# Kernel optimization log

Hardware: AMD Instinct MI355X
Metric: run time of the kernel (lower is better)

Reference implementation:

```python
import jax, jax.numpy as jnp
import numpy as np

L, B, C = 512, 64, 512  # seq_len, batch, tags_size


def setup_inputs() -> dict:
    key = jax.random.key(0)
    k1, k2, k3, k4, k5, k6 = jax.random.split(key, 6)
    std = (1.0 / C) ** 0.5
    emit = jax.random.normal(k1, (L, B, C), dtype=jnp.float32)
    trans = jax.random.normal(k2, (C, C), dtype=jnp.float32) * std
    trans_from_start = jax.random.normal(k3, (C,), dtype=jnp.float32) * std
    trans_to_end = jax.random.normal(k4, (C,), dtype=jnp.float32) * std
    target = jax.random.randint(k5, (L, B), 0, C)
    # left-aligned length mask so mask.sum(0)-1 indexes the last valid step
    lens = jax.random.randint(k6, (B,), L // 2, L + 1)
    mask = jnp.arange(L)[:, None] < lens[None, :]
    return {"emit": emit, "target": target, "mask": mask, "trans": trans,
            "trans_from_start": trans_from_start, "trans_to_end": trans_to_end}


def _log_z(emit, mask, trans, trans_from_start, trans_to_end):
    log_alpha0 = emit[0] + trans_from_start  # (B, C)

    def step(log_alpha, xs):
        e_i, m_i = xs  # (B, C), (B,)
        # scores[b, j] = logsumexp_i( log_alpha[b, i] + trans[i, j] + e_i[b, j] )
        s = jax.nn.logsumexp(log_alpha[:, :, None] + trans[None, :, :] + e_i[:, None, :], axis=1)
        log_alpha = jnp.where(m_i[:, None], s, log_alpha)
        return log_alpha, None

    log_alpha, _ = jax.lax.scan(step, log_alpha0, (emit[1:], mask[1:]))
    return jax.nn.logsumexp(log_alpha + trans_to_end, axis=1).sum()


def _score(emit, target, mask, trans, trans_from_start, trans_to_end):
    l, b, c = emit.shape
    tr = trans[target[:-1], target[1:]]  # (L-1, B)
    scores = jnp.concatenate([jnp.zeros((1, b), emit.dtype), tr], axis=0)
    scores = scores + jnp.take_along_axis(emit, target[:, :, None], axis=2)[..., 0]
    score = jnp.where(mask, scores, jnp.zeros((), emit.dtype)).sum()
    ends = mask.sum(axis=0) - 1  # (B,) index of last valid step
    last_tags = target[ends, jnp.arange(b)]
    score = score + trans_from_start[target[0]].sum() + trans_to_end[last_tags].sum()
    return score


def reference(emit, target, mask, trans, trans_from_start, trans_to_end):
    b = emit.shape[1]
    log_z = _log_z(emit, mask, trans, trans_from_start, trans_to_end)
    score = _score(emit, target, mask, trans, trans_from_start, trans_to_end)
    return (log_z - score) / b
```

## Files before the change

kernel.cpp:

```cpp
#include <hip/hip_runtime.h>
#include <hip/hip_bf16.h>
#include <stdint.h>

#define LL 512
#define BB 64
#define CC 512
#define TM 255

typedef float float4v __attribute__((ext_vector_type(4)));
typedef int   int4v   __attribute__((ext_vector_type(4)));
typedef int   int8v   __attribute__((ext_vector_type(8)));

#define WS_ET     262144
#define WS_SCORE  524288
#define WS_SVA    524292
#define WS_SVB    524548
#define WS_ALPHA  528384
#define WS_BETA   659456


__device__ __forceinline__ bool mask_at(const void* maskp, bool is_byte, int t, int b) {
    if (is_byte) return ((const unsigned char*)maskp)[t * BB + b] != 0;
    return ((const int*)maskp)[t * BB + b] != 0;
}

__device__ __forceinline__ float rowmax16_dpp(float x) {
    int t;
    t = __builtin_amdgcn_update_dpp(0, __float_as_int(x), 0x128, 0xF, 0xF, true);
    x = fmaxf(x, __int_as_float(t));
    t = __builtin_amdgcn_update_dpp(0, __float_as_int(x), 0x124, 0xF, 0xF, true);
    x = fmaxf(x, __int_as_float(t));
    t = __builtin_amdgcn_update_dpp(0, __float_as_int(x), 0x122, 0xF, 0xF, true);
    x = fmaxf(x, __int_as_float(t));
    t = __builtin_amdgcn_update_dpp(0, __float_as_int(x), 0x121, 0xF, 0xF, true);
    x = fmaxf(x, __int_as_float(t));
    return x;
}

__global__ void prep_kernel(const float* __restrict__ trans, unsigned char* __restrict__ ws) {
    int g = blockIdx.x * blockDim.x + threadIdx.x;
    if (g == 0) *(float*)(ws + WS_SCORE) = 0.0f;
    if (g >= 512 * 128) return;
    int n  = g & 511;
    int pd = g >> 9;
    int wv = pd >> 4, rw = pd & 15;
    float f[4], ft[4];
#pragma unroll
    for (int nt = 0; nt < 4; ++nt) {
        int k = 64 * wv + 16 * nt + rw;
        f[nt]  = __expf(trans[(size_t)k * CC + n]);
        ft[nt] = __expf(trans[(size_t)n * CC + k]);
    }
    int r = 0;
    r = __builtin_amdgcn_cvt_pk_fp8_f32(f[0], f[1], r, false);
    r = __builtin_amdgcn_cvt_pk_fp8_f32(f[2], f[3], r, true);
    ((int*)ws)[n * 128 + pd] = r;
    int r2 = 0;
    r2 = __builtin_amdgcn_cvt_pk_fp8_f32(ft[0], ft[1], r2, false);
    r2 = __builtin_amdgcn_cvt_pk_fp8_f32(ft[2], ft[3], r2, true);
    ((int*)(ws + WS_ET))[n * 128 + pd] = r2;
}

__launch_bounds__(512, 2)
__global__ void crf_scan_kernel(const float* __restrict__ emit,
                                const int* __restrict__ target,
                                const void* __restrict__ maskp,
                                const float* __restrict__ trans,
                                const float* __restrict__ tfs,
                                const float* __restrict__ t2e,
                                unsigned char* __restrict__ ws) {
    const int tid = threadIdx.x;
    const bool is_byte = ((const unsigned char*)maskp)[1] != 0;

    if (blockIdx.x >= 8) {
        int sb = blockIdx.x - 8;
        float val = 0.0f;
        for (int e = sb * 512 + tid; e < LL * BB; e += 32 * 512) {
            int t = e >> 6, b = e & 63;
            if (mask_at(maskp, is_byte, t, b)) {
                int tg  = target[t * BB + b];
                float v = emit[(size_t)(t * BB + b) * CC + tg];
                if (t > 0) v += trans[(size_t)target[(t - 1) * BB + b] * CC + tg];
                val += v;
            }
        }
        if (sb == 0 && tid < BB) {
            int b = tid;
            val += tfs[target[b]];
            int lo = 0, hi = LL;
            while (lo < hi) {
                int mid = (lo + hi) >> 1;
                if (mask_at(maskp, is_byte, mid, b)) lo = mid + 1; else hi = mid;
            }
            val += t2e[target[(lo - 1) * BB + b]];
        }
        for (int off = 32; off > 0; off >>= 1) val += __shfl_down(val, off);
        if ((tid & 63) == 0) atomicAdd((float*)(ws + WS_SCORE), val);
        return;
    }

    const bool is_fwd = blockIdx.x < 4;
    const int B0 = (is_fwd ? blockIdx.x : blockIdx.x - 4) * 16;

    __shared__ __align__(16) unsigned char p8[2][16 * 528];
    __shared__ float mslot[4][16];
    __shared__ float Sv[16];
    __shared__ float m0S[16];
    __shared__ float red[16][32];
    __shared__ int   lenS[16];
    __shared__ float mInitS;

    const int wv   = tid >> 6;
    const int lane = tid & 63;
    const int q    = lane >> 4;
    const int r15  = lane & 15;

    const unsigned char* ews = ws + (is_fwd ? 0 : WS_ET);
    int8v ef[4][4];
#pragma unroll
    for (int nt = 0; nt < 4; ++nt) {
        int n = (wv * 4 + nt) * 16 + r15;
#pragma unroll
        for (int kk4 = 0; kk4 < 4; ++kk4) {
            const unsigned char* src = ews + n * 512 + kk4 * 128 + q * 32;
            int4v lo = *(const int4v*)(src);
            int4v hi = *(const int4v*)(src + 16);
            ef[nt][kk4] = __builtin_shufflevector(lo, hi, 0, 1, 2, 3, 4, 5, 6, 7);
        }
    }

    const int c5 = tid >> 5;
    const int s5 = tid & 31;

    if (is_fwd) {
        {
            float lmax = -3.0e38f;
#pragma unroll
            for (int i = 0; i < 4; ++i) {
                int j4 = s5 + 32 * i;
                float4v em = *(const float4v*)(emit + (size_t)(B0 + c5) * CC + 4 * j4);
                float4v tf = *(const float4v*)(tfs + 4 * j4);
                float4v a = em + tf;
                lmax = fmaxf(lmax, fmaxf(fmaxf(a.x, a.y), fmaxf(a.z, a.w)));
            }
            red[c5][s5] = lmax;
        }
        __syncthreads();
        if (tid < 16) {
            float m0 = red[tid][0];
            for (int s = 1; s < 32; ++s) m0 = fmaxf(m0, red[tid][s]);
            Sv[tid]  = m0;
            m0S[tid] = m0;
            mslot[0][tid] = 1.0f;
            mslot[1][tid] = 0.0f;
            mslot[2][tid] = 0.0f;
            mslot[3][tid] = 0.0f;
        }
        __syncthreads();
        {
            float m0 = m0S[c5];
#pragma unroll
            for (int i = 0; i < 4; ++i) {
                int pd = s5 + 32 * i;
                int wvv = pd >> 4, rw = pd & 15;
                float f[4];
#pragma unroll
                for (int nt = 0; nt < 4; ++nt) {
                    int k = 64 * wvv + 16 * nt + rw;
                    f[nt] = __expf(emit[(size_t)(B0 + c5) * CC + k] + tfs[k] - m0);
                }
                int r = 0;
                r = __builtin_amdgcn_cvt_pk_fp8_f32(f[0], f[1], r, false);
                r = __builtin_amdgcn_cvt_pk_fp8_f32(f[2], f[3], r, true);
                *(int*)(&p8[0][0] + c5 * 528 + pd * 4) = r;
            }
        }
        __syncthreads();
    } else {
        {
            float m = t2e[tid];
            for (int off = 32; off > 0; off >>= 1) m = fmaxf(m, __shfl_xor(m, off));
            if (lane == 0) ((float*)red)[wv] = m;
        }
        if (tid < 16) {
            Sv[tid] = 0.0f;
            mslot[0][tid] = 0.0f;
            mslot[1][tid] = 0.0f;
            mslot[2][tid] = 0.0f;
            mslot[3][tid] = 0.0f;
        }
        __syncthreads();
        if (tid == 0) {
            float m = ((float*)red)[0];
            for (int i = 1; i < 8; ++i) m = fmaxf(m, ((float*)red)[i]);
            mInitS = __expf(m);
        }
        __syncthreads();
        {
#pragma unroll
            for (int i = 0; i < 4; ++i) {
                int pd = s5 + 32 * i;
                int wvv = pd >> 4, rw = pd & 15;
                float f[4];
#pragma unroll
                for (int nt = 0; nt < 4; ++nt)
                    f[nt] = __expf(t2e[64 * wvv + 16 * nt + rw]);
                int r = 0;
                r = __builtin_amdgcn_cvt_pk_fp8_f32(f[0], f[1], r, false);
                r = __builtin_amdgcn_cvt_pk_fp8_f32(f[2], f[3], r, true);
                *(int*)(&p8[0][0] + c5 * 528 + pd * 4) = r;
                *(int*)(&p8[1][0] + c5 * 528 + pd * 4) = r;
            }
            int part = 0;
            for (int k = 0; k < 16; ++k)
                part += mask_at(maskp, is_byte, s5 * 16 + k, B0 + c5) ? 1 : 0;
            red[c5][s5] = (float)part;
        }
        __syncthreads();
        if (tid < 16) {
            int s = 0;
            for (int i = 0; i < 32; ++i) s += (int)red[tid][i];
            lenS[tid] = s;
        }
        __syncthreads();
    }

    int lenR[4] = {LL, LL, LL, LL};
    float mInit = 0.0f;
    if (!is_fwd) {
#pragma unroll
        for (int rr = 0; rr < 4; ++rr) lenR[rr] = lenS[q * 4 + rr];
        mInit = mInitS;
    }
    float et2e[4];
#pragma unroll
    for (int nt = 0; nt < 4; ++nt)
        et2e[nt] = __expf(t2e[(wv * 4 + nt) * 16 + r15]);
    float rQ[4] = {1.0f, 1.0f, 1.0f, 1.0f};

    if (is_fwd) {
        const float* eb0 = emit + (size_t)(BB + B0 + q * 4) * CC + (wv * 64 + r15);
        const float* eb1 = eb0 + 2 * CC;
        float ex[16];
#pragma unroll
        for (int nt = 0; nt < 4; ++nt)
#pragma unroll
            for (int rr = 0; rr < 2; ++rr) {
                ex[nt * 4 + rr]     = __expf(eb0[rr * CC + nt * 16]);
                ex[nt * 4 + rr + 2] = __expf(eb1[rr * CC + nt * 16]);
            }

#pragma unroll 2
        for (int t = 1; t <= TM; ++t) {
            const int wp = t & 1;
            const int rp = wp ^ 1;

            const int step = (t < TM) ? (BB * CC) : 0;
            float emn[16];
#pragma unroll
            for (int nt = 0; nt < 4; ++nt)
#pragma unroll
                for (int rr = 0; rr < 2; ++rr) {
                    emn[nt * 4 + rr]     = eb0[step + rr * CC + nt * 16];
                    emn[nt * 4 + rr + 2] = eb1[step + rr * CC + nt * 16];
                }

            int8v af[4];
            const unsigned char* pr = &p8[rp][0] + r15 * 528 + q * 32;
#pragma unroll
            for (int kk4 = 0; kk4 < 4; ++kk4) {
                int4v lo = *(const int4v*)(pr + kk4 * 128);
                int4v hi = *(const int4v*)(pr + kk4 * 128 + 16);
                af[kk4] = __builtin_shufflevector(lo, hi, 0, 1, 2, 3, 4, 5, 6, 7);
            }

            float sig[4], rcv[4];
#pragma unroll
            for (int rr = 0; rr < 4; ++rr) {
                float M1 = mslot[(t - 1) & 3][q * 4 + rr];
                sig[rr] = 64.0f * M1 * rQ[rr];
                rcv[rr] = 1.0f / sig[rr];
                rQ[rr]  = rcv[rr];
            }

            if (wv == 0 && r15 == 0) {
#pragma unroll
                for (int rr = 0; rr < 4; ++rr) mslot[(t + 1) & 3][q * 4 + rr] = 0.0f;
            }

            float4v acc[4];
            const float4v z = {0.f, 0.f, 0.f, 0.f};
#pragma unroll
            for (int nt = 0; nt < 4; ++nt) acc[nt] = z;

#pragma unroll
            for (int kk4 = 0; kk4 < 4; ++kk4)
#pragma unroll
                for (int nt = 0; nt < 2; ++nt)
                    acc[nt] = __builtin_amdgcn_mfma_scale_f32_16x16x128_f8f6f4(
                        af[kk4], ef[nt][kk4], acc[nt],
                        0, 0, 0, 0x7F7F7F7F, 0, 0x7F7F7F7F);

            float exn[16];
#pragma unroll
            for (int i = 0; i < 16; ++i) exn[i] = __expf(emn[i]);

#pragma unroll
            for (int kk4 = 0; kk4 < 4; ++kk4)
#pragma unroll
                for (int nt = 2; nt < 4; ++nt)
                    acc[nt] = __builtin_amdgcn_mfma_scale_f32_16x16x128_f8f6f4(
                        af[kk4], ef[nt][kk4], acc[nt],
                        0, 0, 0, 0x7F7F7F7F, 0, 0x7F7F7F7F);

            float rowmax[4];
#pragma unroll
            for (int rr = 0; rr < 4; ++rr) {
                float v0 = acc[0][rr] * ex[0 * 4 + rr];
                float v1 = acc[1][rr] * ex[1 * 4 + rr];
                acc[0][rr] = v0; acc[1][rr] = v1;
                rowmax[rr] = fmaxf(v0, v1);
            }
#pragma unroll
            for (int rr = 0; rr < 4; ++rr) {
                float v2 = acc[2][rr] * ex[2 * 4 + rr];
                float v3 = acc[3][rr] * ex[3 * 4 + rr];
                acc[2][rr] = v2; acc[3][rr] = v3;
                rowmax[rr] = fmaxf(rowmax[rr], fmaxf(v2, v3));
            }

            {
                unsigned char* wrow = &p8[wp][0] + (wv * 16 + r15) * 4;
#pragma unroll
                for (int rr = 0; rr < 4; ++rr) {
                    float p0 = fminf(acc[0][rr] * rcv[rr], 448.0f);
                    float p1 = fminf(acc[1][rr] * rcv[rr], 448.0f);
                    float p2 = fminf(acc[2][rr] * rcv[rr], 448.0f);
                    float p3 = fminf(acc[3][rr] * rcv[rr], 448.0f);
                    int r = 0;
                    r = __builtin_amdgcn_cvt_pk_fp8_f32(p0, p1, r, false);
                    r = __builtin_amdgcn_cvt_pk_fp8_f32(p2, p3, r, true);
                    *(int*)(wrow + (q * 4 + rr) * 528) = r;
                }
            }

#pragma unroll
            for (int rr = 0; rr < 4; ++rr) {
                float mr = rowmax16_dpp(rowmax[rr]);
                if (r15 == 0)
                    atomicMax((int*)&mslot[t & 3][q * 4 + rr], __float_as_int(mr));
            }

            if (wv == 0 && r15 == 0) {
#pragma unroll
                for (int rr = 0; rr < 4; ++rr) Sv[q * 4 + rr] += __logf(sig[rr]);
            }

            if (t == TM) {
                float* wA = (float*)(ws + WS_ALPHA) + (size_t)(B0 + q * 4) * CC + (wv * 64 + r15);
#pragma unroll
                for (int rr = 0; rr < 4; ++rr)
#pragma unroll
                    for (int nt = 0; nt < 4; ++nt)
                        wA[(size_t)rr * CC + nt * 16] = acc[nt][rr] * rcv[rr];
            }

#pragma unroll
            for (int i = 0; i < 16; ++i) ex[i] = exn[i];
            eb0 += BB * CC;
            eb1 += BB * CC;
            __syncthreads();
        }
        if (tid < 16) ((float*)(ws + WS_SVA))[B0 + tid] = Sv[tid];
    } else {
        const float* eb0 = emit + ((size_t)(LL - 1) * BB + B0 + q * 4) * CC + (wv * 64 + r15);
        const float* eb1 = eb0 + 2 * CC;
        float ex[16];
#pragma unroll
        for (int nt = 0; nt < 4; ++nt)
#pragma unroll
            for (int rr = 0; rr < 2; ++rr) {
                ex[nt * 4 + rr]     = __expf(eb0[rr * CC + nt * 16]);
                ex[nt * 4 + rr + 2] = __expf(eb1[rr * CC + nt * 16]);
            }

#pragma unroll 2
        for (int it = 0; it < 256; ++it) {
            const int t  = 510 - it;
            const int wp = it & 1;
            const int rp = wp ^ 1;

            const int step = (it < 255) ? -(BB * CC) : 0;
            float emn[16];
#pragma unroll
            for (int nt = 0; nt < 4; ++nt)
#pragma unroll
                for (int rr = 0; rr < 2; ++rr) {
                    emn[nt * 4 + rr]     = eb0[step + rr * CC + nt * 16];
                    emn[nt * 4 + rr + 2] = eb1[step + rr * CC + nt * 16];
                }

            int8v af[4];
            const unsigned char* pr = &p8[rp][0] + r15 * 528 + q * 32;
#pragma unroll
            for (int kk4 = 0; kk4 < 4; ++kk4) {
                int4v lo = *(const int4v*)(pr + kk4 * 128);
                int4v hi = *(const int4v*)(pr + kk4 * 128 + 16);
                af[kk4] = __builtin_shufflevector(lo, hi, 0, 1, 2, 3, 4, 5, 6, 7);
            }

            float sig[4], rcv[4];
#pragma unroll
            for (int rr = 0; rr < 4; ++rr) {
                bool ui  = (t >= lenR[rr] - 2);
                float M1 = ui ? mInit : mslot[(it + 3) & 3][q * 4 + rr];
                float rq = ui ? 1.0f : rQ[rr];
                sig[rr] = 64.0f * M1 * rq;
                rcv[rr] = 1.0f / sig[rr];
                rQ[rr]  = rcv[rr];
            }

            if (wv == 0 && r15 == 0) {
#pragma unroll
                for (int rr = 0; rr < 4; ++rr) mslot[(it + 1) & 3][q * 4 + rr] = 0.0f;
            }

            float4v acc[4];
            const float4v z = {0.f, 0.f, 0.f, 0.f};
#pragma unroll
            for (int nt = 0; nt < 4; ++nt) acc[nt] = z;

#pragma unroll
            for (int kk4 = 0; kk4 < 4; ++kk4)
#pragma unroll
                for (int nt = 0; nt < 2; ++nt)
                    acc[nt] = __builtin_amdgcn_mfma_scale_f32_16x16x128_f8f6f4(
                        af[kk4], ef[nt][kk4], acc[nt],
                        0, 0, 0, 0x7F7F7F7F, 0, 0x7F7F7F7F);

            float exn[16];
#pragma unroll
            for (int i = 0; i < 16; ++i) exn[i] = __expf(emn[i]);

#pragma unroll
            for (int kk4 = 0; kk4 < 4; ++kk4)
#pragma unroll
                for (int nt = 2; nt < 4; ++nt)
                    acc[nt] = __builtin_amdgcn_mfma_scale_f32_16x16x128_f8f6f4(
                        af[kk4], ef[nt][kk4], acc[nt],
                        0, 0, 0, 0x7F7F7F7F, 0, 0x7F7F7F7F);

            float rowmax[4];
#pragma unroll
            for (int rr = 0; rr < 4; ++rr) {
                float v0 = acc[0][rr] * ex[0 * 4 + rr];
                float v1 = acc[1][rr] * ex[1 * 4 + rr];
                acc[0][rr] = v0; acc[1][rr] = v1;
                rowmax[rr] = fmaxf(v0, v1);
            }
#pragma unroll
            for (int rr = 0; rr < 4; ++rr) {
                float v2 = acc[2][rr] * ex[2 * 4 + rr];
                float v3 = acc[3][rr] * ex[3 * 4 + rr];
                acc[2][rr] = v2; acc[3][rr] = v3;
                rowmax[rr] = fmaxf(rowmax[rr], fmaxf(v2, v3));
            }

            {
                unsigned char* wrow = &p8[wp][0] + (wv * 16 + r15) * 4;
#pragma unroll
                for (int rr = 0; rr < 4; ++rr) {
                    float p0 = fminf(acc[0][rr] * rcv[rr], 448.0f);
                    float p1 = fminf(acc[1][rr] * rcv[rr], 448.0f);
                    float p2 = fminf(acc[2][rr] * rcv[rr], 448.0f);
                    float p3 = fminf(acc[3][rr] * rcv[rr], 448.0f);
                    int r = 0;
                    r = __builtin_amdgcn_cvt_pk_fp8_f32(p0, p1, r, false);
                    r = __builtin_amdgcn_cvt_pk_fp8_f32(p2, p3, r, true);
                    if (t <= lenR[rr] - 2)
                        *(int*)(wrow + (q * 4 + rr) * 528) = r;
                }
            }

#pragma unroll
            for (int rr = 0; rr < 4; ++rr) {
                float mr = rowmax16_dpp(rowmax[rr]);
                if (r15 == 0)
                    atomicMax((int*)&mslot[it & 3][q * 4 + rr], __float_as_int(mr));
            }

            if (wv == 0 && r15 == 0) {
#pragma unroll
                for (int rr = 0; rr < 4; ++rr)
                    if (t <= lenR[rr] - 2) Sv[q * 4 + rr] += __logf(sig[rr]);
            }

            if (t == TM) {
                float* wB = (float*)(ws + WS_BETA) + (size_t)(B0 + q * 4) * CC + (wv * 64 + r15);
#pragma unroll
                for (int rr = 0; rr < 4; ++rr) {
                    bool live = (t <= lenR[rr] - 2);
#pragma unroll
                    for (int nt = 0; nt < 4; ++nt)
                        wB[(size_t)rr * CC + nt * 16] = live ? (acc[nt][rr] * rcv[rr]) : et2e[nt];
                }
            }

#pragma unroll
            for (int i = 0; i < 16; ++i) ex[i] = exn[i];
            eb0 -= BB * CC;
            eb1 -= BB * CC;
            __syncthreads();
        }
        if (tid < 16) ((float*)(ws + WS_SVB))[B0 + tid] = Sv[tid];
    }
}

__global__ void combine_kernel(const unsigned char* __restrict__ ws, float* __restrict__ out) {
    __shared__ float acc8[8];
    const int tid = threadIdx.x;
    const int c  = tid >> 3;
    const int s8 = tid & 7;
    const float* A = (const float*)(ws + WS_ALPHA) + (size_t)c * CC;
    const float* B = (const float*)(ws + WS_BETA)  + (size_t)c * CC;
    float d = 0.0f;
    for (int i = s8; i < CC; i += 8) d += A[i] * B[i];
    d += __shfl_xor(d, 1);
    d += __shfl_xor(d, 2);
    d += __shfl_xor(d, 4);
    float v = 0.0f;
    if (s8 == 0)
        v = ((const float*)(ws + WS_SVA))[c] + ((const float*)(ws + WS_SVB))[c] + __logf(d);
    for (int off = 32; off > 0; off >>= 1) v += __shfl_down(v, off);
    if ((tid & 63) == 0) acc8[tid >> 6] = v;
    __syncthreads();
    if (tid == 0) {
        float s = 0.0f;
        for (int i = 0; i < 8; ++i) s += acc8[i];
        out[0] = (s - *(const float*)(ws + WS_SCORE)) * (1.0f / 64.0f);
    }
}

extern "C" void kernel_launch(void* const* d_in, const int* in_sizes, int n_in,
                              void* d_out, int out_size, void* d_ws, size_t ws_size,
                              hipStream_t stream) {
    const float* emit   = (const float*)d_in[0];
    const int*   target = (const int*)d_in[1];
    const void*  maskp  = d_in[2];
    const float* trans  = (const float*)d_in[3];
    const float* tfs    = (const float*)d_in[4];
    const float* t2e    = (const float*)d_in[5];
    unsigned char* ws   = (unsigned char*)d_ws;
    float* out          = (float*)d_out;

    prep_kernel<<<256, 256, 0, stream>>>(trans, ws);
    crf_scan_kernel<<<40, 512, 0, stream>>>(emit, target, maskp, trans, tfs, t2e, ws);
    combine_kernel<<<1, 512, 0, stream>>>(ws, out);
}
```

Baseline: 534.1 us.

## Split scan columns across 16 waves with 1024-thread blocks

The forward and backward scan blocks now launch 1024 threads instead of 512, so each wave owns 32 output columns (2 MFMA tiles) instead of 64. This halves the dependent MFMA chain and the exp work each wave does per time step. To match the new column ownership, the fp8 probability write-back uses a remapped byte offset with 2-byte stores, and the score reduction blocks are resized to 16 blocks of 1024 threads. The cost is a block-wide barrier across twice as many waves every step, higher per-block register pressure under the new launch bounds, and loop unrolling is turned off.

```diff
diff --git a/kernel.cpp b/kernel.cpp
--- a/kernel.cpp
+++ b/kernel.cpp
@@ -61,7 +61,7 @@
     ((int*)(ws + WS_ET))[n * 128 + pd] = r2;
 }
 
-__launch_bounds__(512, 2)
+__launch_bounds__(1024, 1)
 __global__ void crf_scan_kernel(const float* __restrict__ emit,
                                 const int* __restrict__ target,
                                 const void* __restrict__ maskp,
@@ -75,7 +75,7 @@
     if (blockIdx.x >= 8) {
         int sb = blockIdx.x - 8;
         float val = 0.0f;
-        for (int e = sb * 512 + tid; e < LL * BB; e += 32 * 512) {
+        for (int e = sb * 1024 + tid; e < LL * BB; e += 16 * 1024) {
             int t = e >> 6, b = e & 63;
             if (mask_at(maskp, is_byte, t, b)) {
                 int tg  = target[t * BB + b];
@@ -116,10 +116,10 @@
     const int r15  = lane & 15;
 
     const unsigned char* ews = ws + (is_fwd ? 0 : WS_ET);
-    int8v ef[4][4];
-#pragma unroll
-    for (int nt = 0; nt < 4; ++nt) {
-        int n = (wv * 4 + nt) * 16 + r15;
+    int8v ef[2][4];
+#pragma unroll
+    for (int nt = 0; nt < 2; ++nt) {
+        int n = wv * 32 + nt * 16 + r15;
 #pragma unroll
         for (int kk4 = 0; kk4 < 4; ++kk4) {
             const unsigned char* src = ews + n * 512 + kk4 * 128 + q * 32;
@@ -133,7 +133,7 @@
     const int s5 = tid & 31;
 
     if (is_fwd) {
-        {
+        if (tid < 512) {
             float lmax = -3.0e38f;
 #pragma unroll
             for (int i = 0; i < 4; ++i) {
@@ -157,7 +157,7 @@
             mslot[3][tid] = 0.0f;
         }
         __syncthreads();
-        {
+        if (tid < 512) {
             float m0 = m0S[c5];
 #pragma unroll
             for (int i = 0; i < 4; ++i) {
@@ -177,7 +177,7 @@
         }
         __syncthreads();
     } else {
-        {
+        if (tid < 512) {
             float m = t2e[tid];
             for (int off = 32; off > 0; off >>= 1) m = fmaxf(m, __shfl_xor(m, off));
             if (lane == 0) ((float*)red)[wv] = m;
@@ -196,7 +196,7 @@
             mInitS = __expf(m);
         }
         __syncthreads();
-        {
+        if (tid < 512) {
 #pragma unroll
             for (int i = 0; i < 4; ++i) {
                 int pd = s5 + 32 * i;
@@ -225,54 +225,42 @@
         __syncthreads();
     }
 
-    int lenR[4] = {LL, LL, LL, LL};
-    float mInit = 0.0f;
-    if (!is_fwd) {
-#pragma unroll
-        for (int rr = 0; rr < 4; ++rr) lenR[rr] = lenS[q * 4 + rr];
-        mInit = mInitS;
-    }
-    float et2e[4];
-#pragma unroll
-    for (int nt = 0; nt < 4; ++nt)
-        et2e[nt] = __expf(t2e[(wv * 4 + nt) * 16 + r15]);
     float rQ[4] = {1.0f, 1.0f, 1.0f, 1.0f};
+    const int wcol = (wv >> 1) * 64 + r15 * 4 + (wv & 1) * 2;
 
     if (is_fwd) {
-        const float* eb0 = emit + (size_t)(BB + B0 + q * 4) * CC + (wv * 64 + r15);
+        const float* eb0 = emit + (size_t)(BB + B0 + q * 4) * CC + (wv * 32 + r15);
         const float* eb1 = eb0 + 2 * CC;
-        float ex[16];
-#pragma unroll
-        for (int nt = 0; nt < 4; ++nt)
+        float ex[8];
+#pragma unroll
+        for (int nt = 0; nt < 2; ++nt)
 #pragma unroll
             for (int rr = 0; rr < 2; ++rr) {
                 ex[nt * 4 + rr]     = __expf(eb0[rr * CC + nt * 16]);
                 ex[nt * 4 + rr + 2] = __expf(eb1[rr * CC + nt * 16]);
             }
 
-#pragma unroll 2
+#pragma unroll 1
         for (int t = 1; t <= TM; ++t) {
             const int wp = t & 1;
             const int rp = wp ^ 1;
 
             const int step = (t < TM) ? (BB * CC) : 0;
-            float emn[16];
-#pragma unroll
-            for (int nt = 0; nt < 4; ++nt)
+            float emn[8];
+#pragma unroll
+            for (int nt = 0; nt < 2; ++nt)
 #pragma unroll
                 for (int rr = 0; rr < 2; ++rr) {
                     emn[nt * 4 + rr]     = eb0[step + rr * CC + nt * 16];
                     emn[nt * 4 + rr + 2] = eb1[step + rr * CC + nt * 16];
                 }
 
-            int8v af[4];
             const unsigned char* pr = &p8[rp][0] + r15 * 528 + q * 32;
-#pragma unroll
-            for (int kk4 = 0; kk4 < 4; ++kk4) {
-                int4v lo = *(const int4v*)(pr + kk4 * 128);
-                int4v hi = *(const int4v*)(pr + kk4 * 128 + 16);
-                af[kk4] = __builtin_shufflevector(lo, hi, 0, 1, 2, 3, 4, 5, 6, 7);
-            }
+            int8v af0, af1, af2, af3;
+            { int4v lo = *(const int4v*)(pr + 0 * 128); int4v hi = *(const int4v*)(pr + 0 * 128 + 16);
+              af0 = __builtin_shufflevector(lo, hi, 0, 1, 2, 3, 4, 5, 6, 7); }
+            { int4v lo = *(const int4v*)(pr + 1 * 128); int4v hi = *(const int4v*)(pr + 1 * 128 + 16);
+              af1 = __builtin_shufflevector(lo, hi, 0, 1, 2, 3, 4, 5, 6, 7); }
 
             float sig[4], rcv[4];
 #pragma unroll
@@ -282,65 +270,48 @@
                 rcv[rr] = 1.0f / sig[rr];
                 rQ[rr]  = rcv[rr];
             }
-
             if (wv == 0 && r15 == 0) {
 #pragma unroll
                 for (int rr = 0; rr < 4; ++rr) mslot[(t + 1) & 3][q * 4 + rr] = 0.0f;
             }
 
-            float4v acc[4];
             const float4v z = {0.f, 0.f, 0.f, 0.f};
-#pragma unroll
-            for (int nt = 0; nt < 4; ++nt) acc[nt] = z;
-
-#pragma unroll
-            for (int kk4 = 0; kk4 < 4; ++kk4)
-#pragma unroll
-                for (int nt = 0; nt < 2; ++nt)
-                    acc[nt] = __builtin_amdgcn_mfma_scale_f32_16x16x128_f8f6f4(
-                        af[kk4], ef[nt][kk4], acc[nt],
-                        0, 0, 0, 0x7F7F7F7F, 0, 0x7F7F7F7F);
-
-            float exn[16];
-#pragma unroll
-            for (int i = 0; i < 16; ++i) exn[i] = __expf(emn[i]);
-
-#pragma unroll
-            for (int kk4 = 0; kk4 < 4; ++kk4)
-#pragma unroll
-                for (int nt = 2; nt < 4; ++nt)
-                    acc[nt] = __builtin_amdgcn_mfma_scale_f32_16x16x128_f8f6f4(
-                        af[kk4], ef[nt][kk4], acc[nt],
-                        0, 0, 0, 0x7F7F7F7F, 0, 0x7F7F7F7F);
+            float4v acc0 = z, acc1 = z;
+            acc0 = __builtin_amdgcn_mfma_scale_f32_16x16x128_f8f6f4(af0, ef[0][0], acc0, 0, 0, 0, 0x7F7F7F7F, 0, 0x7F7F7F7F);
+            acc1 = __builtin_amdgcn_mfma_scale_f32_16x16x128_f8f6f4(af0, ef[1][0], acc1, 0, 0, 0, 0x7F7F7F7F, 0, 0x7F7F7F7F);
+            { int4v lo = *(const int4v*)(pr + 2 * 128); int4v hi = *(const int4v*)(pr + 2 * 128 + 16);
+              af2 = __builtin_shufflevector(lo, hi, 0, 1, 2, 3, 4, 5, 6, 7); }
+            { int4v lo = *(const int4v*)(pr + 3 * 128); int4v hi = *(const int4v*)(pr + 3 * 128 + 16);
+              af3 = __builtin_shufflevector(lo, hi, 0, 1, 2, 3, 4, 5, 6, 7); }
+            acc0 = __builtin_amdgcn_mfma_scale_f32_16x16x128_f8f6f4(af1, ef[0][1], acc0, 0, 0, 0, 0x7F7F7F7F, 0, 0x7F7F7F7F);
+            acc1 = __builtin_amdgcn_mfma_scale_f32_16x16x128_f8f6f4(af1, ef[1][1], acc1, 0, 0, 0, 0x7F7F7F7F, 0, 0x7F7F7F7F);
+
+            float exn[8];
+#pragma unroll
+            for (int i = 0; i < 8; ++i) exn[i] = __expf(emn[i]);
+
+            acc0 = __builtin_amdgcn_mfma_scale_f32_16x16x128_f8f6f4(af2, ef[0][2], acc0, 0, 0, 0, 0x7F7F7F7F, 0, 0x7F7F7F7F);
+            acc1 = __builtin_amdgcn_mfma_scale_f32_16x16x128_f8f6f4(af2, ef[1][2], acc1, 0, 0, 0, 0x7F7F7F7F, 0, 0x7F7F7F7F);
+            acc0 = __builtin_amdgcn_mfma_scale_f32_16x16x128_f8f6f4(af3, ef[0][3], acc0, 0, 0, 0, 0x7F7F7F7F, 0, 0x7F7F7F7F);
+            acc1 = __builtin_amdgcn_mfma_scale_f32_16x16x128_f8f6f4(af3, ef[1][3], acc1, 0, 0, 0, 0x7F7F7F7F, 0, 0x7F7F7F7F);
 
             float rowmax[4];
 #pragma unroll
             for (int rr = 0; rr < 4; ++rr) {
-                float v0 = acc[0][rr] * ex[0 * 4 + rr];
-                float v1 = acc[1][rr] * ex[1 * 4 + rr];
-                acc[0][rr] = v0; acc[1][rr] = v1;
+                float v0 = acc0[rr] * ex[rr];
+                float v1 = acc1[rr] * ex[4 + rr];
+                acc0[rr] = v0; acc1[rr] = v1;
                 rowmax[rr] = fmaxf(v0, v1);
             }
-#pragma unroll
-            for (int rr = 0; rr < 4; ++rr) {
-                float v2 = acc[2][rr] * ex[2 * 4 + rr];
-                float v3 = acc[3][rr] * ex[3 * 4 + rr];
-                acc[2][rr] = v2; acc[3][rr] = v3;
-                rowmax[rr] = fmaxf(rowmax[rr], fmaxf(v2, v3));
-            }
 
             {
-                unsigned char* wrow = &p8[wp][0] + (wv * 16 + r15) * 4;
+                unsigned char* wbase = &p8[wp][0] + wcol;
 #pragma unroll
                 for (int rr = 0; rr < 4; ++rr) {
-                    float p0 = fminf(acc[0][rr] * rcv[rr], 448.0f);
-                    float p1 = fminf(acc[1][rr] * rcv[rr], 448.0f);
-                    float p2 = fminf(acc[2][rr] * rcv[rr], 448.0f);
-                    float p3 = fminf(acc[3][rr] * rcv[rr], 448.0f);
-                    int r = 0;
-                    r = __builtin_amdgcn_cvt_pk_fp8_f32(p0, p1, r, false);
-                    r = __builtin_amdgcn_cvt_pk_fp8_f32(p2, p3, r, true);
-                    *(int*)(wrow + (q * 4 + rr) * 528) = r;
+                    float p0 = fminf(acc0[rr] * rcv[rr], 448.0f);
+                    float p1 = fminf(acc1[rr] * rcv[rr], 448.0f);
+                    int r = __builtin_amdgcn_cvt_pk_fp8_f32(p0, p1, 0, false);
+                    *(short*)(wbase + (q * 4 + rr) * 528) = (short)r;
                 }
             }
 
@@ -357,57 +328,60 @@
             }
 
             if (t == TM) {
-                float* wA = (float*)(ws + WS_ALPHA) + (size_t)(B0 + q * 4) * CC + (wv * 64 + r15);
-#pragma unroll
-                for (int rr = 0; rr < 4; ++rr)
-#pragma unroll
-                    for (int nt = 0; nt < 4; ++nt)
-                        wA[(size_t)rr * CC + nt * 16] = acc[nt][rr] * rcv[rr];
-            }
-
-#pragma unroll
-            for (int i = 0; i < 16; ++i) ex[i] = exn[i];
+                float* wA = (float*)(ws + WS_ALPHA) + (size_t)(B0 + q * 4) * CC + (wv * 32 + r15);
+#pragma unroll
+                for (int rr = 0; rr < 4; ++rr) {
+                    wA[(size_t)rr * CC + 0]  = acc0[rr] * rcv[rr];
+                    wA[(size_t)rr * CC + 16] = acc1[rr] * rcv[rr];
+                }
+            }
+
+#pragma unroll
+            for (int i = 0; i < 8; ++i) ex[i] = exn[i];
             eb0 += BB * CC;
             eb1 += BB * CC;
             __syncthreads();
         }
         if (tid < 16) ((float*)(ws + WS_SVA))[B0 + tid] = Sv[tid];
     } else {
-        const float* eb0 = emit + ((size_t)(LL - 1) * BB + B0 + q * 4) * CC + (wv * 64 + r15);
+        int lenR[4];
+        float mInit = mInitS;
+#pragma unroll
+        for (int rr = 0; rr < 4; ++rr) lenR[rr] = lenS[q * 4 + rr];
+
+        const float* eb0 = emit + ((size_t)(LL - 1) * BB + B0 + q * 4) * CC + (wv * 32 + r15);
         const float* eb1 = eb0 + 2 * CC;
-        float ex[16];
-#pragma unroll
-        for (int nt = 0; nt < 4; ++nt)
+        float ex[8];
+#pragma unroll
+        for (int nt = 0; nt < 2; ++nt)
 #pragma unroll
             for (int rr = 0; rr < 2; ++rr) {
                 ex[nt * 4 + rr]     = __expf(eb0[rr * CC + nt * 16]);
                 ex[nt * 4 + rr + 2] = __expf(eb1[rr * CC + nt * 16]);
             }
 
-#pragma unroll 2
+#pragma unroll 1
         for (int it = 0; it < 256; ++it) {
             const int t  = 510 - it;
             const int wp = it & 1;
             const int rp = wp ^ 1;
 
             const int step = (it < 255) ? -(BB * CC) : 0;
-            float emn[16];
-#pragma unroll
-            for (int nt = 0; nt < 4; ++nt)
+            float emn[8];
+#pragma unroll
+            for (int nt = 0; nt < 2; ++nt)
 #pragma unroll
                 for (int rr = 0; rr < 2; ++rr) {
                     emn[nt * 4 + rr]     = eb0[step + rr * CC + nt * 16];
                     emn[nt * 4 + rr + 2] = eb1[step + rr * CC + nt * 16];
                 }
 
-            int8v af[4];
             const unsigned char* pr = &p8[rp][0] + r15 * 528 + q * 32;
-#pragma unroll
-            for (int kk4 = 0; kk4 < 4; ++kk4) {
-                int4v lo = *(const int4v*)(pr + kk4 * 128);
-                int4v hi = *(const int4v*)(pr + kk4 * 128 + 16);
-                af[kk4] = __builtin_shufflevector(lo, hi, 0, 1, 2, 3, 4, 5, 6, 7);
-            }
+            int8v af0, af1, af2, af3;
+            { int4v lo = *(const int4v*)(pr + 0 * 128); int4v hi = *(const int4v*)(pr + 0 * 128 + 16);
+              af0 = __builtin_shufflevector(lo, hi, 0, 1, 2, 3, 4, 5, 6, 7); }
+            { int4v lo = *(const int4v*)(pr + 1 * 128); int4v hi = *(const int4v*)(pr + 1 * 128 + 16);
+              af1 = __builtin_shufflevector(lo, hi, 0, 1, 2, 3, 4, 5, 6, 7); }
 
             float sig[4], rcv[4];
 #pragma unroll
@@ -419,66 +393,49 @@
                 rcv[rr] = 1.0f / sig[rr];
                 rQ[rr]  = rcv[rr];
             }
-
             if (wv == 0 && r15 == 0) {
 #pragma unroll
                 for (int rr = 0; rr < 4; ++rr) mslot[(it + 1) & 3][q * 4 + rr] = 0.0f;
             }
 
-            float4v acc[4];
             const float4v z = {0.f, 0.f, 0.f, 0.f};
-#pragma unroll
-            for (int nt = 0; nt < 4; ++nt) acc[nt] = z;
-
-#pragma unroll
-            for (int kk4 = 0; kk4 < 4; ++kk4)
-#pragma unroll
-                for (int nt = 0; nt < 2; ++nt)
-                    acc[nt] = __builtin_amdgcn_mfma_scale_f32_16x16x128_f8f6f4(
-                        af[kk4], ef[nt][kk4], acc[nt],
-                        0, 0, 0, 0x7F7F7F7F, 0, 0x7F7F7F7F);
-
-            float exn[16];
-#pragma unroll
-            for (int i = 0; i < 16; ++i) exn[i] = __expf(emn[i]);
-
-#pragma unroll
-            for (int kk4 = 0; kk4 < 4; ++kk4)
-#pragma unroll
-                for (int nt = 2; nt < 4; ++nt)
-                    acc[nt] = __builtin_amdgcn_mfma_scale_f32_16x16x128_f8f6f4(
-                        af[kk4], ef[nt][kk4], acc[nt],
-                        0, 0, 0, 0x7F7F7F7F, 0, 0x7F7F7F7F);
+            float4v acc0 = z, acc1 = z;
+            acc0 = __builtin_amdgcn_mfma_scale_f32_16x16x128_f8f6f4(af0, ef[0][0], acc0, 0, 0, 0, 0x7F7F7F7F, 0, 0x7F7F7F7F);
+            acc1 = __builtin_amdgcn_mfma_scale_f32_16x16x128_f8f6f4(af0, ef[1][0], acc1, 0, 0, 0, 0x7F7F7F7F, 0, 0x7F7F7F7F);
+            { int4v lo = *(const int4v*)(pr + 2 * 128); int4v hi = *(const int4v*)(pr + 2 * 128 + 16);
+              af2 = __builtin_shufflevector(lo, hi, 0, 1, 2, 3, 4, 5, 6, 7); }
+            { int4v lo = *(const int4v*)(pr + 3 * 128); int4v hi = *(const int4v*)(pr + 3 * 128 + 16);
+              af3 = __builtin_shufflevector(lo, hi, 0, 1, 2, 3, 4, 5, 6, 7); }
+            acc0 = __builtin_amdgcn_mfma_scale_f32_16x16x128_f8f6f4(af1, ef[0][1], acc0, 0, 0, 0, 0x7F7F7F7F, 0, 0x7F7F7F7F);
+            acc1 = __builtin_amdgcn_mfma_scale_f32_16x16x128_f8f6f4(af1, ef[1][1], acc1, 0, 0, 0, 0x7F7F7F7F, 0, 0x7F7F7F7F);
+
+            float exn[8];
+#pragma unroll
+            for (int i = 0; i < 8; ++i) exn[i] = __expf(emn[i]);
+
+            acc0 = __builtin_amdgcn_mfma_scale_f32_16x16x128_f8f6f4(af2, ef[0][2], acc0, 0, 0, 0, 0x7F7F7F7F, 0, 0x7F7F7F7F);
+            acc1 = __builtin_amdgcn_mfma_scale_f32_16x16x128_f8f6f4(af2, ef[1][2], acc1, 0, 0, 0, 0x7F7F7F7F, 0, 0x7F7F7F7F);
+            acc0 = __builtin_amdgcn_mfma_scale_f32_16x16x128_f8f6f4(af3, ef[0][3], acc0, 0, 0, 0, 0x7F7F7F7F, 0, 0x7F7F7F7F);
+            acc1 = __builtin_amdgcn_mfma_scale_f32_16x16x128_f8f6f4(af3, ef[1][3], acc1, 0, 0, 0, 0x7F7F7F7F, 0, 0x7F7F7F7F);
 
             float rowmax[4];
 #pragma unroll
             for (int rr = 0; rr < 4; ++rr) {
-                float v0 = acc[0][rr] * ex[0 * 4 + rr];
-                float v1 = acc[1][rr] * ex[1 * 4 + rr];
-                acc[0][rr] = v0; acc[1][rr] = v1;
+                float v0 = acc0[rr] * ex[rr];
+                float v1 = acc1[rr] * ex[4 + rr];
+                acc0[rr] = v0; acc1[rr] = v1;
                 rowmax[rr] = fmaxf(v0, v1);
             }
-#pragma unroll
-            for (int rr = 0; rr < 4; ++rr) {
-                float v2 = acc[2][rr] * ex[2 * 4 + rr];
-                float v3 = acc[3][rr] * ex[3 * 4 + rr];
-                acc[2][rr] = v2; acc[3][rr] = v3;
-                rowmax[rr] = fmaxf(rowmax[rr], fmaxf(v2, v3));
-            }
 
             {
-                unsigned char* wrow = &p8[wp][0] + (wv * 16 + r15) * 4;
+                unsigned char* wbase = &p8[wp][0] + wcol;
 #pragma unroll
                 for (int rr = 0; rr < 4; ++rr) {
-                    float p0 = fminf(acc[0][rr] * rcv[rr], 448.0f);
-                    float p1 = fminf(acc[1][rr] * rcv[rr], 448.0f);
-                    float p2 = fminf(acc[2][rr] * rcv[rr], 448.0f);
-                    float p3 = fminf(acc[3][rr] * rcv[rr], 448.0f);
-                    int r = 0;
-                    r = __builtin_amdgcn_cvt_pk_fp8_f32(p0, p1, r, false);
-                    r = __builtin_amdgcn_cvt_pk_fp8_f32(p2, p3, r, true);
+                    float p0 = fminf(acc0[rr] * rcv[rr], 448.0f);
+                    float p1 = fminf(acc1[rr] * rcv[rr], 448.0f);
+                    int r = __builtin_amdgcn_cvt_pk_fp8_f32(p0, p1, 0, false);
                     if (t <= lenR[rr] - 2)
-                        *(int*)(wrow + (q * 4 + rr) * 528) = r;
+                        *(short*)(wbase + (q * 4 + rr) * 528) = (short)r;
                 }
             }
 
@@ -496,18 +453,19 @@
             }
 
             if (t == TM) {
-                float* wB = (float*)(ws + WS_BETA) + (size_t)(B0 + q * 4) * CC + (wv * 64 + r15);
+                float* wB = (float*)(ws + WS_BETA) + (size_t)(B0 + q * 4) * CC + (wv * 32 + r15);
+                float e0 = __expf(t2e[wv * 32 + r15]);
+                float e1 = __expf(t2e[wv * 32 + 16 + r15]);
 #pragma unroll
                 for (int rr = 0; rr < 4; ++rr) {
                     bool live = (t <= lenR[rr] - 2);
-#pragma unroll
-                    for (int nt = 0; nt < 4; ++nt)
-                        wB[(size_t)rr * CC + nt * 16] = live ? (acc[nt][rr] * rcv[rr]) : et2e[nt];
-                }
-            }
-
-#pragma unroll
-            for (int i = 0; i < 16; ++i) ex[i] = exn[i];
+                    wB[(size_t)rr * CC + 0]  = live ? (acc0[rr] * rcv[rr]) : e0;
+                    wB[(size_t)rr * CC + 16] = live ? (acc1[rr] * rcv[rr]) : e1;
+                }
+            }
+
+#pragma unroll
+            for (int i = 0; i < 8; ++i) ex[i] = exn[i];
             eb0 -= BB * CC;
             eb1 -= BB * CC;
             __syncthreads();
@@ -554,6 +512,6 @@
     float* out          = (float*)d_out;
 
     prep_kernel<<<256, 256, 0, stream>>>(trans, ws);
-    crf_scan_kernel<<<40, 512, 0, stream>>>(emit, target, maskp, trans, tfs, t2e, ws);
+    crf_scan_kernel<<<24, 1024, 0, stream>>>(emit, target, maskp, trans, tfs, t2e, ws);
     combine_kernel<<<1, 512, 0, stream>>>(ws, out);
 }
```

After: 1.119 ms. 110% more time.

## Use power-of-two exponent rescaling and a lighter barrier in the CRF recurrence

Applied to the files above, without the earlier changes.

Replaces the per-step float rescale (reciprocal of 64*max times the previous factor, plus a logf accumulated in shared memory) with a power-of-two scale built directly from the max's exponent bits. The log-normaliser is kept as an integer exponent sum in registers. It also vectorises the elementwise scale, clamp and max work, moves the emission pointer advance and load ahead, and swaps __syncthreads for a custom lgkmcnt-wait plus s_barrier. This removes a division, a log and shared-memory traffic from the serial critical path. The cost is coarser scaling granularity, which changes the fp8 range usage, and a hand-rolled barrier that depends on correct wait-count semantics.

```diff
diff --git a/kernel.cpp b/kernel.cpp
--- a/kernel.cpp
+++ b/kernel.cpp
@@ -35,6 +35,26 @@
     t = __builtin_amdgcn_update_dpp(0, __float_as_int(x), 0x121, 0xF, 0xF, true);
     x = fmaxf(x, __int_as_float(t));
     return x;
+}
+
+__device__ __forceinline__ float4v vmax4(float4v a, float4v b) {
+    float4v r;
+    r[0] = fmaxf(a[0], b[0]); r[1] = fmaxf(a[1], b[1]);
+    r[2] = fmaxf(a[2], b[2]); r[3] = fmaxf(a[3], b[3]);
+    return r;
+}
+__device__ __forceinline__ float4v vmin4s(float4v a, float c) {
+    float4v r;
+    r[0] = fminf(a[0], c); r[1] = fminf(a[1], c);
+    r[2] = fminf(a[2], c); r[3] = fminf(a[3], c);
+    return r;
+}
+
+__device__ __forceinline__ void step_barrier() {
+    asm volatile("s_waitcnt lgkmcnt(0)" ::: "memory");
+    __builtin_amdgcn_sched_barrier(0);
+    __builtin_amdgcn_s_barrier();
+    asm volatile("" ::: "memory");
 }
 
 __global__ void prep_kernel(const float* __restrict__ trans, unsigned char* __restrict__ ws) {
@@ -103,8 +123,7 @@
     const int B0 = (is_fwd ? blockIdx.x : blockIdx.x - 4) * 16;
 
     __shared__ __align__(16) unsigned char p8[2][16 * 528];
-    __shared__ float mslot[4][16];
-    __shared__ float Sv[16];
+    __shared__ __align__(16) float mslot[4][16];
     __shared__ float m0S[16];
     __shared__ float red[16][32];
     __shared__ int   lenS[16];
@@ -149,7 +168,6 @@
         if (tid < 16) {
             float m0 = red[tid][0];
             for (int s = 1; s < 32; ++s) m0 = fmaxf(m0, red[tid][s]);
-            Sv[tid]  = m0;
             m0S[tid] = m0;
             mslot[0][tid] = 1.0f;
             mslot[1][tid] = 0.0f;
@@ -183,7 +201,6 @@
             if (lane == 0) ((float*)red)[wv] = m;
         }
         if (tid < 16) {
-            Sv[tid] = 0.0f;
             mslot[0][tid] = 0.0f;
             mslot[1][tid] = 0.0f;
             mslot[2][tid] = 0.0f;
@@ -225,73 +242,59 @@
         __syncthreads();
     }
 
-    int lenR[4] = {LL, LL, LL, LL};
-    float mInit = 0.0f;
-    if (!is_fwd) {
-#pragma unroll
-        for (int rr = 0; rr < 4; ++rr) lenR[rr] = lenS[q * 4 + rr];
-        mInit = mInitS;
-    }
-    float et2e[4];
-#pragma unroll
-    for (int nt = 0; nt < 4; ++nt)
-        et2e[nt] = __expf(t2e[(wv * 4 + nt) * 16 + r15]);
-    float rQ[4] = {1.0f, 1.0f, 1.0f, 1.0f};
+    int4v gsum = {0, 0, 0, 0};
+    const float4v z4 = {0.f, 0.f, 0.f, 0.f};
 
     if (is_fwd) {
         const float* eb0 = emit + (size_t)(BB + B0 + q * 4) * CC + (wv * 64 + r15);
         const float* eb1 = eb0 + 2 * CC;
-        float ex[16];
-#pragma unroll
-        for (int nt = 0; nt < 4; ++nt)
-#pragma unroll
-            for (int rr = 0; rr < 2; ++rr) {
-                ex[nt * 4 + rr]     = __expf(eb0[rr * CC + nt * 16]);
-                ex[nt * 4 + rr + 2] = __expf(eb1[rr * CC + nt * 16]);
-            }
+        float4v ex4[4];
+#pragma unroll
+        for (int nt = 0; nt < 4; ++nt) {
+            ex4[nt][0] = __expf(eb0[0 * CC + nt * 16]);
+            ex4[nt][1] = __expf(eb0[1 * CC + nt * 16]);
+            ex4[nt][2] = __expf(eb1[0 * CC + nt * 16]);
+            ex4[nt][3] = __expf(eb1[1 * CC + nt * 16]);
+        }
 
 #pragma unroll 2
         for (int t = 1; t <= TM; ++t) {
             const int wp = t & 1;
             const int rp = wp ^ 1;
-
-            const int step = (t < TM) ? (BB * CC) : 0;
-            float emn[16];
-#pragma unroll
-            for (int nt = 0; nt < 4; ++nt)
-#pragma unroll
-                for (int rr = 0; rr < 2; ++rr) {
-                    emn[nt * 4 + rr]     = eb0[step + rr * CC + nt * 16];
-                    emn[nt * 4 + rr + 2] = eb1[step + rr * CC + nt * 16];
-                }
-
+            eb0 += BB * CC;
+            eb1 += BB * CC;
+
+            const unsigned char* pr = &p8[rp][0] + r15 * 528 + q * 32;
             int8v af[4];
-            const unsigned char* pr = &p8[rp][0] + r15 * 528 + q * 32;
 #pragma unroll
             for (int kk4 = 0; kk4 < 4; ++kk4) {
                 int4v lo = *(const int4v*)(pr + kk4 * 128);
                 int4v hi = *(const int4v*)(pr + kk4 * 128 + 16);
                 af[kk4] = __builtin_shufflevector(lo, hi, 0, 1, 2, 3, 4, 5, 6, 7);
             }
-
-            float sig[4], rcv[4];
-#pragma unroll
-            for (int rr = 0; rr < 4; ++rr) {
-                float M1 = mslot[(t - 1) & 3][q * 4 + rr];
-                sig[rr] = 64.0f * M1 * rQ[rr];
-                rcv[rr] = 1.0f / sig[rr];
-                rQ[rr]  = rcv[rr];
-            }
-
-            if (wv == 0 && r15 == 0) {
-#pragma unroll
-                for (int rr = 0; rr < 4; ++rr) mslot[(t + 1) & 3][q * 4 + rr] = 0.0f;
-            }
+            int4v me = *(const int4v*)&mslot[(t - 1) & 3][q * 4];
+
+            float4v emn4[4];
+#pragma unroll
+            for (int nt = 0; nt < 4; ++nt) {
+                emn4[nt][0] = eb0[0 * CC + nt * 16];
+                emn4[nt][1] = eb0[1 * CC + nt * 16];
+                emn4[nt][2] = eb1[0 * CC + nt * 16];
+                emn4[nt][3] = eb1[1 * CC + nt * 16];
+            }
+
+            int4v e4 = me >> 23;
+            int4v s2b = (248 - e4) << 23;
+            float4v s24;
+            s24[0] = __int_as_float(s2b[0]); s24[1] = __int_as_float(s2b[1]);
+            s24[2] = __int_as_float(s2b[2]); s24[3] = __int_as_float(s2b[3]);
+
+            if (wv == 0 && r15 == 0)
+                *(float4v*)&mslot[(t + 1) & 3][q * 4] = z4;
 
             float4v acc[4];
-            const float4v z = {0.f, 0.f, 0.f, 0.f};
-#pragma unroll
-            for (int nt = 0; nt < 4; ++nt) acc[nt] = z;
+#pragma unroll
+            for (int nt = 0; nt < 4; ++nt) acc[nt] = z4;
 
 #pragma unroll
             for (int kk4 = 0; kk4 < 4; ++kk4)
@@ -301,9 +304,14 @@
                         af[kk4], ef[nt][kk4], acc[nt],
                         0, 0, 0, 0x7F7F7F7F, 0, 0x7F7F7F7F);
 
-            float exn[16];
-#pragma unroll
-            for (int i = 0; i < 16; ++i) exn[i] = __expf(emn[i]);
+            float4v exn4[4];
+#pragma unroll
+            for (int nt = 0; nt < 4; ++nt) {
+                exn4[nt][0] = __expf(emn4[nt][0]);
+                exn4[nt][1] = __expf(emn4[nt][1]);
+                exn4[nt][2] = __expf(emn4[nt][2]);
+                exn4[nt][3] = __expf(emn4[nt][3]);
+            }
 
 #pragma unroll
             for (int kk4 = 0; kk4 < 4; ++kk4)
@@ -313,122 +321,117 @@
                         af[kk4], ef[nt][kk4], acc[nt],
                         0, 0, 0, 0x7F7F7F7F, 0, 0x7F7F7F7F);
 
-            float rowmax[4];
+            float4v p4[4];
+#pragma unroll
+            for (int nt = 0; nt < 4; ++nt) {
+                float4v exr = ex4[nt] * s24;
+                p4[nt] = acc[nt] * exr;
+            }
+
+            if (t == TM) {
+                float* wA = (float*)(ws + WS_ALPHA) + (size_t)(B0 + q * 4) * CC + (wv * 64 + r15);
+#pragma unroll
+                for (int nt = 0; nt < 4; ++nt)
+#pragma unroll
+                    for (int rr = 0; rr < 4; ++rr)
+                        wA[(size_t)rr * CC + nt * 16] = p4[nt][rr];
+            }
+
+            float4v rm4 = vmax4(vmax4(p4[0], p4[1]), vmax4(p4[2], p4[3]));
 #pragma unroll
             for (int rr = 0; rr < 4; ++rr) {
-                float v0 = acc[0][rr] * ex[0 * 4 + rr];
-                float v1 = acc[1][rr] * ex[1 * 4 + rr];
-                acc[0][rr] = v0; acc[1][rr] = v1;
-                rowmax[rr] = fmaxf(v0, v1);
-            }
-#pragma unroll
-            for (int rr = 0; rr < 4; ++rr) {
-                float v2 = acc[2][rr] * ex[2 * 4 + rr];
-                float v3 = acc[3][rr] * ex[3 * 4 + rr];
-                acc[2][rr] = v2; acc[3][rr] = v3;
-                rowmax[rr] = fmaxf(rowmax[rr], fmaxf(v2, v3));
+                float mr = rowmax16_dpp(rm4[rr]);
+                if (r15 == 0)
+                    atomicMax((int*)&mslot[t & 3][q * 4 + rr], __float_as_int(mr));
             }
 
             {
                 unsigned char* wrow = &p8[wp][0] + (wv * 16 + r15) * 4;
+                float4v pc[4];
+#pragma unroll
+                for (int nt = 0; nt < 4; ++nt) pc[nt] = vmin4s(p4[nt], 448.0f);
 #pragma unroll
                 for (int rr = 0; rr < 4; ++rr) {
-                    float p0 = fminf(acc[0][rr] * rcv[rr], 448.0f);
-                    float p1 = fminf(acc[1][rr] * rcv[rr], 448.0f);
-                    float p2 = fminf(acc[2][rr] * rcv[rr], 448.0f);
-                    float p3 = fminf(acc[3][rr] * rcv[rr], 448.0f);
                     int r = 0;
-                    r = __builtin_amdgcn_cvt_pk_fp8_f32(p0, p1, r, false);
-                    r = __builtin_amdgcn_cvt_pk_fp8_f32(p2, p3, r, true);
+                    r = __builtin_amdgcn_cvt_pk_fp8_f32(pc[0][rr], pc[1][rr], r, false);
+                    r = __builtin_amdgcn_cvt_pk_fp8_f32(pc[2][rr], pc[3][rr], r, true);
                     *(int*)(wrow + (q * 4 + rr) * 528) = r;
                 }
             }
 
-#pragma unroll
-            for (int rr = 0; rr < 4; ++rr) {
-                float mr = rowmax16_dpp(rowmax[rr]);
-                if (r15 == 0)
-                    atomicMax((int*)&mslot[t & 3][q * 4 + rr], __float_as_int(mr));
-            }
-
-            if (wv == 0 && r15 == 0) {
-#pragma unroll
-                for (int rr = 0; rr < 4; ++rr) Sv[q * 4 + rr] += __logf(sig[rr]);
-            }
-
-            if (t == TM) {
-                float* wA = (float*)(ws + WS_ALPHA) + (size_t)(B0 + q * 4) * CC + (wv * 64 + r15);
-#pragma unroll
-                for (int rr = 0; rr < 4; ++rr)
-#pragma unroll
-                    for (int nt = 0; nt < 4; ++nt)
-                        wA[(size_t)rr * CC + nt * 16] = acc[nt][rr] * rcv[rr];
-            }
-
-#pragma unroll
-            for (int i = 0; i < 16; ++i) ex[i] = exn[i];
-            eb0 += BB * CC;
-            eb1 += BB * CC;
-            __syncthreads();
-        }
-        if (tid < 16) ((float*)(ws + WS_SVA))[B0 + tid] = Sv[tid];
+            if (wv == 0 && r15 == 0) gsum += (e4 - 121);
+
+#pragma unroll
+            for (int nt = 0; nt < 4; ++nt) ex4[nt] = exn4[nt];
+            step_barrier();
+        }
+        if (wv == 0 && r15 == 0) {
+#pragma unroll
+            for (int rr = 0; rr < 4; ++rr)
+                ((float*)(ws + WS_SVA))[B0 + q * 4 + rr] =
+                    m0S[q * 4 + rr] + 0.6931471805599453f * (float)gsum[rr];
+        }
     } else {
+        int lenR[4];
+#pragma unroll
+        for (int rr = 0; rr < 4; ++rr) lenR[rr] = lenS[q * 4 + rr];
+        const int eInit = __float_as_int(mInitS) >> 23;
+
         const float* eb0 = emit + ((size_t)(LL - 1) * BB + B0 + q * 4) * CC + (wv * 64 + r15);
         const float* eb1 = eb0 + 2 * CC;
-        float ex[16];
-#pragma unroll
-        for (int nt = 0; nt < 4; ++nt)
-#pragma unroll
-            for (int rr = 0; rr < 2; ++rr) {
-                ex[nt * 4 + rr]     = __expf(eb0[rr * CC + nt * 16]);
-                ex[nt * 4 + rr + 2] = __expf(eb1[rr * CC + nt * 16]);
-            }
+        float4v ex4[4];
+#pragma unroll
+        for (int nt = 0; nt < 4; ++nt) {
+            ex4[nt][0] = __expf(eb0[0 * CC + nt * 16]);
+            ex4[nt][1] = __expf(eb0[1 * CC + nt * 16]);
+            ex4[nt][2] = __expf(eb1[0 * CC + nt * 16]);
+            ex4[nt][3] = __expf(eb1[1 * CC + nt * 16]);
+        }
 
 #pragma unroll 2
         for (int it = 0; it < 256; ++it) {
             const int t  = 510 - it;
             const int wp = it & 1;
             const int rp = wp ^ 1;
-
-            const int step = (it < 255) ? -(BB * CC) : 0;
-            float emn[16];
-#pragma unroll
-            for (int nt = 0; nt < 4; ++nt)
-#pragma unroll
-                for (int rr = 0; rr < 2; ++rr) {
-                    emn[nt * 4 + rr]     = eb0[step + rr * CC + nt * 16];
-                    emn[nt * 4 + rr + 2] = eb1[step + rr * CC + nt * 16];
-                }
-
+            eb0 -= BB * CC;
+            eb1 -= BB * CC;
+
+            const unsigned char* pr = &p8[rp][0] + r15 * 528 + q * 32;
             int8v af[4];
-            const unsigned char* pr = &p8[rp][0] + r15 * 528 + q * 32;
 #pragma unroll
             for (int kk4 = 0; kk4 < 4; ++kk4) {
                 int4v lo = *(const int4v*)(pr + kk4 * 128);
                 int4v hi = *(const int4v*)(pr + kk4 * 128 + 16);
                 af[kk4] = __builtin_shufflevector(lo, hi, 0, 1, 2, 3, 4, 5, 6, 7);
             }
-
-            float sig[4], rcv[4];
+            int4v me = *(const int4v*)&mslot[(it + 3) & 3][q * 4];
+
+            float4v emn4[4];
+#pragma unroll
+            for (int nt = 0; nt < 4; ++nt) {
+                emn4[nt][0] = eb0[0 * CC + nt * 16];
+                emn4[nt][1] = eb0[1 * CC + nt * 16];
+                emn4[nt][2] = eb1[0 * CC + nt * 16];
+                emn4[nt][3] = eb1[1 * CC + nt * 16];
+            }
+
+            int4v e4 = me >> 23;
+            int4v eU;
+            float4v s2U;
 #pragma unroll
             for (int rr = 0; rr < 4; ++rr) {
-                bool ui  = (t >= lenR[rr] - 2);
-                float M1 = ui ? mInit : mslot[(it + 3) & 3][q * 4 + rr];
-                float rq = ui ? 1.0f : rQ[rr];
-                sig[rr] = 64.0f * M1 * rq;
-                rcv[rr] = 1.0f / sig[rr];
-                rQ[rr]  = rcv[rr];
-            }
-
-            if (wv == 0 && r15 == 0) {
-#pragma unroll
-                for (int rr = 0; rr < 4; ++rr) mslot[(it + 1) & 3][q * 4 + rr] = 0.0f;
-            }
+                bool ui = (t >= lenR[rr] - 2);
+                int e = ui ? eInit : e4[rr];
+                eU[rr] = e;
+                s2U[rr] = __int_as_float((248 - e) << 23);
+            }
+
+            if (wv == 0 && r15 == 0)
+                *(float4v*)&mslot[(it + 1) & 3][q * 4] = z4;
 
             float4v acc[4];
-            const float4v z = {0.f, 0.f, 0.f, 0.f};
-#pragma unroll
-            for (int nt = 0; nt < 4; ++nt) acc[nt] = z;
+#pragma unroll
+            for (int nt = 0; nt < 4; ++nt) acc[nt] = z4;
 
 #pragma unroll
             for (int kk4 = 0; kk4 < 4; ++kk4)
@@ -438,9 +441,14 @@
                         af[kk4], ef[nt][kk4], acc[nt],
                         0, 0, 0, 0x7F7F7F7F, 0, 0x7F7F7F7F);
 
-            float exn[16];
-#pragma unroll
-            for (int i = 0; i < 16; ++i) exn[i] = __expf(emn[i]);
+            float4v exn4[4];
+#pragma unroll
+            for (int nt = 0; nt < 4; ++nt) {
+                exn4[nt][0] = __expf(emn4[nt][0]);
+                exn4[nt][1] = __expf(emn4[nt][1]);
+                exn4[nt][2] = __expf(emn4[nt][2]);
+                exn4[nt][3] = __expf(emn4[nt][3]);
+            }
 
 #pragma unroll
             for (int kk4 = 0; kk4 < 4; ++kk4)
@@ -450,69 +458,63 @@
                         af[kk4], ef[nt][kk4], acc[nt],
                         0, 0, 0, 0x7F7F7F7F, 0, 0x7F7F7F7F);
 
-            float rowmax[4];
+            float4v p4[4];
+#pragma unroll
+            for (int nt = 0; nt < 4; ++nt) {
+                float4v exr = ex4[nt] * s2U;
+                p4[nt] = acc[nt] * exr;
+            }
+
+            if (t == TM) {
+                float* wB = (float*)(ws + WS_BETA) + (size_t)(B0 + q * 4) * CC + (wv * 64 + r15);
+#pragma unroll
+                for (int nt = 0; nt < 4; ++nt) {
+                    float e2 = __expf(t2e[wv * 64 + nt * 16 + r15]);
+#pragma unroll
+                    for (int rr = 0; rr < 4; ++rr)
+                        wB[(size_t)rr * CC + nt * 16] = (t <= lenR[rr] - 2) ? p4[nt][rr] : e2;
+                }
+            }
+
+            float4v rm4 = vmax4(vmax4(p4[0], p4[1]), vmax4(p4[2], p4[3]));
 #pragma unroll
             for (int rr = 0; rr < 4; ++rr) {
-                float v0 = acc[0][rr] * ex[0 * 4 + rr];
-                float v1 = acc[1][rr] * ex[1 * 4 + rr];
-                acc[0][rr] = v0; acc[1][rr] = v1;
-                rowmax[rr] = fmaxf(v0, v1);
-            }
-#pragma unroll
-            for (int rr = 0; rr < 4; ++rr) {
-                float v2 = acc[2][rr] * ex[2 * 4 + rr];
-                float v3 = acc[3][rr] * ex[3 * 4 + rr];
-                acc[2][rr] = v2; acc[3][rr] = v3;
-                rowmax[rr] = fmaxf(rowmax[rr], fmaxf(v2, v3));
+                float mr = rowmax16_dpp(rm4[rr]);
+                if (r15 == 0)
+                    atomicMax((int*)&mslot[it & 3][q * 4 + rr], __float_as_int(mr));
             }
 
             {
                 unsigned char* wrow = &p8[wp][0] + (wv * 16 + r15) * 4;
+                float4v pc[4];
+#pragma unroll
+                for (int nt = 0; nt < 4; ++nt) pc[nt] = vmin4s(p4[nt], 448.0f);
 #pragma unroll
                 for (int rr = 0; rr < 4; ++rr) {
-                    float p0 = fminf(acc[0][rr] * rcv[rr], 448.0f);
-                    float p1 = fminf(acc[1][rr] * rcv[rr], 448.0f);
-                    float p2 = fminf(acc[2][rr] * rcv[rr], 448.0f);
-                    float p3 = fminf(acc[3][rr] * rcv[rr], 448.0f);
                     int r = 0;
-                    r = __builtin_amdgcn_cvt_pk_fp8_f32(p0, p1, r, false);
-                    r = __builtin_amdgcn_cvt_pk_fp8_f32(p2, p3, r, true);
+                    r = __builtin_amdgcn_cvt_pk_fp8_f32(pc[0][rr], pc[1][rr], r, false);
+                    r = __builtin_amdgcn_cvt_pk_fp8_f32(pc[2][rr], pc[3][rr], r, true);
                     if (t <= lenR[rr] - 2)
                         *(int*)(wrow + (q * 4 + rr) * 528) = r;
                 }
             }
 
-#pragma unroll
-            for (int rr = 0; rr < 4; ++rr) {
-                float mr = rowmax16_dpp(rowmax[rr]);
-                if (r15 == 0)
-                    atomicMax((int*)&mslot[it & 3][q * 4 + rr], __float_as_int(mr));
-            }
-
             if (wv == 0 && r15 == 0) {
 #pragma unroll
                 for (int rr = 0; rr < 4; ++rr)
-                    if (t <= lenR[rr] - 2) Sv[q * 4 + rr] += __logf(sig[rr]);
-            }
-
-            if (t == TM) {
-                float* wB = (float*)(ws + WS_BETA) + (size_t)(B0 + q * 4) * CC + (wv * 64 + r15);
-#pragma unroll
-                for (int rr = 0; rr < 4; ++rr) {
-                    bool live = (t <= lenR[rr] - 2);
-#pragma unroll
-                    for (int nt = 0; nt < 4; ++nt)
-                        wB[(size_t)rr * CC + nt * 16] = live ? (acc[nt][rr] * rcv[rr]) : et2e[nt];
-                }
-            }
-
-#pragma unroll
-            for (int i = 0; i < 16; ++i) ex[i] = exn[i];
-            eb0 -= BB * CC;
-            eb1 -= BB * CC;
-            __syncthreads();
-        }
-        if (tid < 16) ((float*)(ws + WS_SVB))[B0 + tid] = Sv[tid];
+                    if (t <= lenR[rr] - 2) gsum[rr] += (eU[rr] - 121);
+            }
+
+#pragma unroll
+            for (int nt = 0; nt < 4; ++nt) ex4[nt] = exn4[nt];
+            step_barrier();
+        }
+        if (wv == 0 && r15 == 0) {
+#pragma unroll
+            for (int rr = 0; rr < 4; ++rr)
+                ((float*)(ws + WS_SVB))[B0 + q * 4 + rr] =
+                    0.6931471805599453f * (float)gsum[rr];
+        }
     }
 }
 
```

New measurement: 495.4 us. -7.2%, faster.
